# Kernel optimization log

Measured on AMD Instinct MI355X. Metric: run time of the kernel, lower is better.

The kernel has to match this reference:

```python
import jax, jax.numpy as jnp
import numpy as np

D_MODEL = 1024
N_HEADS = 16
D_HEAD = 64
D_MLP = 4096
EPS = 1e-5
IGNORE = -1e5
ATTN_SCALE = float(np.sqrt(D_HEAD))


def setup_inputs() -> dict:
    key = jax.random.key(0)
    ks = jax.random.split(key, 10)
    s = 0.02
    return {
        "x": jax.random.normal(ks[0], (2, 2048, D_MODEL), jnp.float32),
        "ln1_w": jnp.ones((D_MODEL,), jnp.float32),
        "ln1_b": jnp.zeros((D_MODEL,), jnp.float32),
        "W_Q": jax.random.normal(ks[1], (N_HEADS, D_MODEL, D_HEAD), jnp.float32) * s,
        "W_K": jax.random.normal(ks[2], (N_HEADS, D_MODEL, D_HEAD), jnp.float32) * s,
        "W_V": jax.random.normal(ks[3], (N_HEADS, D_MODEL, D_HEAD), jnp.float32) * s,
        "W_O": jax.random.normal(ks[4], (N_HEADS, D_HEAD, D_MODEL), jnp.float32) * s,
        "b_Q": jnp.zeros((N_HEADS, D_HEAD), jnp.float32),
        "b_K": jnp.zeros((N_HEADS, D_HEAD), jnp.float32),
        "b_V": jnp.zeros((N_HEADS, D_HEAD), jnp.float32),
        "b_O": jnp.zeros((D_MODEL,), jnp.float32),
        "ln2_w": jnp.ones((D_MODEL,), jnp.float32),
        "ln2_b": jnp.zeros((D_MODEL,), jnp.float32),
        "W_in": jax.random.normal(ks[5], (D_MODEL, D_MLP), jnp.float32) * s,
        "b_in": jnp.zeros((D_MLP,), jnp.float32),
        "W_out": jax.random.normal(ks[6], (D_MLP, D_MODEL), jnp.float32) * s,
        "b_out": jnp.zeros((D_MODEL,), jnp.float32),
    }


def layer_norm(x, w, b):
    x = x - x.mean(axis=-1, keepdims=True)
    scale = jnp.sqrt((x * x).mean(axis=-1, keepdims=True) + EPS)
    return (x / scale) * w + b


def attention(x, W_Q, W_K, W_V, W_O, b_Q, b_K, b_V, b_O):
    # x: [b, s, d_model]; W_{Q,K,V}: [h, d_model, d_head]
    q = jnp.einsum('bsm,hmd->bshd', x, W_Q) + b_Q
    k = jnp.einsum('bsm,hmd->bshd', x, W_K) + b_K
    v = jnp.einsum('bsm,hmd->bshd', x, W_V) + b_V
    scores = jnp.einsum('bqhd,bkhd->bhqk', q, k) / ATTN_SCALE
    s = x.shape[1]
    mask = jnp.tril(jnp.ones((s, s), bool))  # causal
    scores = jnp.where(mask, scores, IGNORE)
    attn = jax.nn.softmax(scores, axis=-1)
    z = jnp.einsum('bkhd,bhqk->bqhd', v, attn)
    return jnp.einsum('bqhd,hdm->bqm', z, W_O) + b_O


def mlp(x, W_in, b_in, W_out, b_out):
    pre = jnp.einsum('bsm,mf->bsf', x, W_in) + b_in
    post = jax.nn.gelu(pre, approximate=False)
    return jnp.einsum('bsf,fm->bsm', post, W_out) + b_out


def reference(x, ln1_w, ln1_b, W_Q, W_K, W_V, W_O, b_Q, b_K, b_V, b_O,
              ln2_w, ln2_b, W_in, b_in, W_out, b_out):
    resid = x + attention(layer_norm(x, ln1_w, ln1_b), W_Q, W_K, W_V, W_O,
                          b_Q, b_K, b_V, b_O)
    out = resid + mlp(layer_norm(resid, ln2_w, ln2_b), W_in, b_in, W_out, b_out)
    return out
```

## Files before the change

### kernel.cpp

```cpp
#include <hip/hip_runtime.h>

typedef __attribute__((ext_vector_type(4))) float f32x4;
typedef __attribute__((ext_vector_type(8))) __bf16 bf16x8;
typedef __attribute__((ext_vector_type(8))) unsigned short ushort8;
typedef __attribute__((ext_vector_type(4))) unsigned short ushort4v;

union UBF8 { ushort8 u; bf16x8 b; };
static __device__ __forceinline__ bf16x8 as_bf(ushort8 v) { UBF8 x; x.u = v; return x.b; }

static __device__ __forceinline__ unsigned short f2bf(float f) {
  union { __bf16 h; unsigned short u; } v; v.h = (__bf16)f; return v.u;
}

static __device__ __forceinline__ unsigned short f2bf_rn(float f) {
  union { float f; unsigned u; } v; v.f = f;
  unsigned r = v.u + 0x7fffu + ((v.u >> 16) & 1u);
  return (unsigned short)(r >> 16);
}

static __device__ __forceinline__ bf16x8 scale8(ushort8 u, float c) {
  ushort8 r;
#pragma unroll
  for (int j = 0; j < 8; j++) {
    union { unsigned u; float f; } t; t.u = ((unsigned)u[j]) << 16;
    r[j] = f2bf_rn(t.f * c);
  }
  return as_bf(r);
}

static __device__ __forceinline__ float gelu_f(float x) {
  return 0.5f * x * (1.0f + erff(x * 0.70710678118654752f));
}

typedef const __attribute__((address_space(1))) void* gas_p;
typedef __attribute__((address_space(3))) void* las_p;
static __device__ __forceinline__ void gload16(const void* g, void* l) {
  __builtin_amdgcn_global_load_lds((gas_p)g, (las_p)l, 16, 0, 0);
}

__global__ __launch_bounds__(256) void ln_kernel(
    const float* __restrict__ in, const float* __restrict__ w,
    const float* __restrict__ b, unsigned short* __restrict__ out)
{
  const int row = blockIdx.x, t = threadIdx.x;
  const float4 v = *reinterpret_cast<const float4*>(in + (size_t)row * 1024 + t * 4);
  float s = v.x + v.y + v.z + v.w;
#pragma unroll
  for (int o = 32; o >= 1; o >>= 1) s += __shfl_xor(s, o);
  __shared__ float ps[4], qs[4];
  if ((t & 63) == 0) ps[t >> 6] = s;
  __syncthreads();
  const float mean = (ps[0] + ps[1] + ps[2] + ps[3]) * (1.0f / 1024.0f);
  const float cx = v.x - mean, cy = v.y - mean, cz = v.z - mean, cw = v.w - mean;
  float q = cx * cx + cy * cy + cz * cz + cw * cw;
#pragma unroll
  for (int o = 32; o >= 1; o >>= 1) q += __shfl_xor(q, o);
  if ((t & 63) == 0) qs[t >> 6] = q;
  __syncthreads();
  const float rstd = rsqrtf((qs[0] + qs[1] + qs[2] + qs[3]) * (1.0f / 1024.0f) + 1e-5f);
  const float4 wv = *reinterpret_cast<const float4*>(w + t * 4);
  const float4 bv = *reinterpret_cast<const float4*>(b + t * 4);
  ushort4v o4;
  o4.x = f2bf(cx * rstd * wv.x + bv.x);
  o4.y = f2bf(cy * rstd * wv.y + bv.y);
  o4.z = f2bf(cz * rstd * wv.z + bv.z);
  o4.w = f2bf(cw * rstd * wv.w + bv.w);
  *reinterpret_cast<ushort4v*>(out + (size_t)row * 1024 + t * 4) = o4;
}

__global__ __launch_bounds__(256) void conv_qkv_kernel(
    const float* __restrict__ WQ, const float* __restrict__ WK,
    const float* __restrict__ WV, unsigned short* __restrict__ out)
{
  __shared__ float t[32][33];
  const int mat_h = blockIdx.z;
  const int mat = mat_h >> 4, h = mat_h & 15;
  const float* W = (mat == 0 ? WQ : (mat == 1 ? WK : WV)) + (size_t)h * (1024 * 64);
  const int m0 = blockIdx.x * 32;
  const int d0 = blockIdx.y * 32;
  const int tx = threadIdx.x & 31, ty = threadIdx.x >> 5;
#pragma unroll
  for (int j = 0; j < 4; j++)
    t[ty + j * 8][tx] = W[(size_t)(m0 + ty + j * 8) * 64 + d0 + tx];
  __syncthreads();
  const size_t obase = (size_t)(mat * 1024 + h * 64 + d0);
#pragma unroll
  for (int j = 0; j < 4; j++)
    out[(obase + ty + j * 8) * 1024 + m0 + tx] = f2bf(t[tx][ty + j * 8]);
}

__global__ __launch_bounds__(256) void pack_bias_kernel(
    const float* __restrict__ bQ, const float* __restrict__ bK,
    const float* __restrict__ bV, float* __restrict__ out)
{
  const int i = blockIdx.x * 256 + threadIdx.x;
  if (i < 1024) out[i] = bQ[i];
  else if (i < 2048) out[i] = bK[i - 1024];
  else if (i < 3072) out[i] = bV[i - 2048];
}

__global__ __launch_bounds__(256) void transpose_cast_kernel(
    const float* __restrict__ in, unsigned short* __restrict__ out, int R, int C)
{
  __shared__ float t[32][33];
  const int c0 = blockIdx.x * 32, r0 = blockIdx.y * 32;
  const int tx = threadIdx.x & 31, ty = threadIdx.x >> 5;
#pragma unroll
  for (int j = 0; j < 4; j++)
    t[ty + j * 8][tx] = in[(size_t)(r0 + ty + j * 8) * C + c0 + tx];
  __syncthreads();
#pragma unroll
  for (int j = 0; j < 4; j++)
    out[(size_t)(c0 + ty + j * 8) * R + r0 + tx] = f2bf(t[tx][ty + j * 8]);
}

template <int BN, int EPI, int WAVES>
__global__ __launch_bounds__(WAVES * 64) void gemm_kernel(
    const unsigned short* __restrict__ A, const unsigned short* __restrict__ Bt,
    void* Cout, const float* __restrict__ bias, const float* resid,
    int N, int K, int gx)
{
  constexpr int BM = 128, BK = 64;
  constexpr int NF = (BN * 2) / (WAVES * 16);
  constexpr int CA = (BM / 8) / WAVES;
  constexpr int CB = (BN / 8) / WAVES;
  __shared__ __align__(16) unsigned short As[2][BM * BK];
  __shared__ __align__(16) unsigned short Bs[2][BN * BK];
  const int tid = threadIdx.x, lane = tid & 63, w = tid >> 6;
  const int nwg = gridDim.x;
  int id = blockIdx.x;
  id = (id & 7) * (nwg >> 3) + (id >> 3);
  const int bm = (id % gx) * BM, bn = (id / gx) * BN;

  const int l15 = lane & 15, hi = lane >> 4;
  const int arow = (w >> 2) * 64;
  const int brow = (w & 3) * (BN / 4);
  f32x4 acc[4][NF] = {};

  const int srow = lane >> 3;
  const int scol = ((lane & 7) ^ srow) * 8;
  const unsigned short* Ag[CA];
  const unsigned short* Bg[CB];
#pragma unroll
  for (int it = 0; it < CA; it++)
    Ag[it] = A + (size_t)(bm + 8 * (it * WAVES + w) + srow) * K + scol;
#pragma unroll
  for (int it = 0; it < CB; it++)
    Bg[it] = Bt + (size_t)(bn + 8 * (it * WAVES + w) + srow) * K + scol;

  const int rsw = (l15 & 7) << 4;
  const int NT = K / BK;

  auto stage = [&](int k0, int buf) {
#pragma unroll
    for (int it = 0; it < CA; it++)
      gload16(Ag[it] + k0, &As[buf][(it * WAVES + w) * 512]);
#pragma unroll
    for (int it = 0; it < CB; it++)
      gload16(Bg[it] + k0, &Bs[buf][(it * WAVES + w) * 512]);
  };

  stage(0, 0);
  __syncthreads();
  int cur = 0;

  for (int t = 0; t < NT; ++t) {
    if (t + 1 < NT) stage((t + 1) * BK, cur ^ 1);

    const char* Asb = (const char*)As[cur];
    const char* Bsb = (const char*)Bs[cur];
    bf16x8 af[2][4], bfr[2][NF];
#pragma unroll
    for (int kk = 0; kk < 2; kk++) {
      const int cb = kk * 64 + hi * 16;
#pragma unroll
      for (int mf = 0; mf < 4; mf++) {
        const int R = arow + mf * 16 + l15;
        af[kk][mf] = as_bf(*reinterpret_cast<const ushort8*>(Asb + R * (BK * 2) + (cb ^ rsw)));
      }
#pragma unroll
      for (int nf = 0; nf < NF; nf++) {
        const int R = brow + nf * 16 + l15;
        bfr[kk][nf] = as_bf(*reinterpret_cast<const ushort8*>(Bsb + R * (BK * 2) + (cb ^ rsw)));
      }
    }
#pragma unroll
    for (int kk = 0; kk < 2; kk++)
#pragma unroll
      for (int mf = 0; mf < 4; mf++)
#pragma unroll
        for (int nf = 0; nf < NF; nf++)
          acc[mf][nf] = __builtin_amdgcn_mfma_f32_16x16x32_bf16(af[kk][mf], bfr[kk][nf], acc[mf][nf], 0, 0, 0);

    __syncthreads();
    cur ^= 1;
  }

  const int row0 = bm + arow + 4 * hi;
  const int col0 = bn + brow + l15;
#pragma unroll
  for (int mf = 0; mf < 4; mf++) {
#pragma unroll
    for (int nf = 0; nf < NF; nf++) {
#pragma unroll
      for (int i = 0; i < 4; i++) {
        const int row = row0 + mf * 16 + i;
        const int col = col0 + nf * 16;
        float v = acc[mf][nf][i] + bias[col];
        if (EPI == 1) v += resid[(size_t)row * N + col];
        if (EPI == 2) v = gelu_f(v);
        if (EPI == 1) ((float*)Cout)[(size_t)row * N + col] = v;
        else          ((unsigned short*)Cout)[(size_t)row * N + col] = f2bf(v);
      }
    }
  }
}

__global__ __launch_bounds__(256) void attn_kernel(
    const unsigned short* __restrict__ qkv, unsigned short* __restrict__ zout)
{
  __shared__ __align__(16) unsigned short Ks[64 * 72];
  __shared__ __align__(16) unsigned short Vt[64 * 72];
  __shared__ __align__(16) unsigned short Ps[4 * 16 * 72];
  const int tid = threadIdx.x, lane = tid & 63, w = tid >> 6;
  const int l15 = lane & 15, hi = lane >> 4, ko = hi * 8;
  const int j = blockIdx.x, bh = blockIdx.y;
  const int cA = j, cB = 31 - j;
  const size_t tok0 = (size_t)(bh >> 4) * 2048;
  const int h = bh & 15;
  const int qoff = h * 64, koff = 1024 + h * 64, voff = 2048 + h * 64;
  const int rowA = cA * 64 + w * 16;
  const int rowB = cB * 64 + w * 16;
  const float qscale = 0.125f * 1.44269504f;

  bf16x8 qfA[2], qfB[2];
#pragma unroll
  for (int kf = 0; kf < 2; kf++) {
    qfA[kf] = scale8(*reinterpret_cast<const ushort8*>(qkv + (tok0 + rowA + l15) * 3072 + qoff + kf * 32 + ko), qscale);
    qfB[kf] = scale8(*reinterpret_cast<const ushort8*>(qkv + (tok0 + rowB + l15) * 3072 + qoff + kf * 32 + ko), qscale);
  }

  float mA[4], lA[4], mB[4], lB[4];
  f32x4 zA[4], zB[4];
#pragma unroll
  for (int i = 0; i < 4; i++) {
    mA[i] = -1e30f; lA[i] = 0.0f; mB[i] = -1e30f; lB[i] = 0.0f;
#pragma unroll
    for (int nf = 0; nf < 4; nf++) { zA[nf][i] = 0.0f; zB[nf][i] = 0.0f; }
  }

  unsigned short* Pw = Ps + w * (16 * 72);
  const int sr = tid >> 3, scol = (tid & 7) * 8;

  for (int kt = 0; kt <= cB; kt++) {
    __syncthreads();
#pragma unroll
    for (int it = 0; it < 2; it++) {
      const int rr = sr + it * 32;
      const size_t gb = (tok0 + kt * 64 + rr) * 3072;
      *reinterpret_cast<ushort8*>(&Ks[rr * 72 + scol]) =
          *reinterpret_cast<const ushort8*>(qkv + gb + koff + scol);
      ushort8 vv = *reinterpret_cast<const ushort8*>(qkv + gb + voff + scol);
#pragma unroll
      for (int jj = 0; jj < 8; jj++) {
        const int d = scol + jj;
        Vt[d * 72 + (rr ^ (((d >> 3) & 7) << 3))] = vv[jj];
      }
    }
    __syncthreads();

    bf16x8 kb[4][2], vb[4][2];
#pragma unroll
    for (int nf = 0; nf < 4; nf++)
#pragma unroll
      for (int kf = 0; kf < 2; kf++) {
        kb[nf][kf] = as_bf(*reinterpret_cast<const ushort8*>(&Ks[(nf * 16 + l15) * 72 + kf * 32 + ko]));
        const int d = nf * 16 + l15;
        vb[nf][kf] = as_bf(*reinterpret_cast<const ushort8*>(
            &Vt[d * 72 + ((kf * 32 + ko) ^ (((d >> 3) & 7) << 3))]));
      }

    const bool actA = (kt <= cA);

    f32x4 sA[4] = {}, sB[4] = {};
    __builtin_amdgcn_s_setprio(1);
#pragma unroll
    for (int nf = 0; nf < 4; nf++)
#pragma unroll
      for (int kf = 0; kf < 2; kf++) {
        if (actA) sA[nf] = __builtin_amdgcn_mfma_f32_16x16x32_bf16(qfA[kf], kb[nf][kf], sA[nf], 0, 0, 0);
        sB[nf] = __builtin_amdgcn_mfma_f32_16x16x32_bf16(qfB[kf], kb[nf][kf], sB[nf], 0, 0, 0);
      }
    __builtin_amdgcn_s_setprio(0);

    auto process = [&](f32x4* s, float* mrow, float* lrow, f32x4* accz, int rowbase, bool dm) {
#pragma unroll
      for (int i = 0; i < 4; i++) {
        const int rg = rowbase + 4 * hi + i;
        float mx = -1e30f;
#pragma unroll
        for (int nf = 0; nf < 4; nf++) {
          float v = s[nf][i];
          if (dm && (kt * 64 + nf * 16 + l15 > rg)) v = -1e30f;
          s[nf][i] = v;
          mx = fmaxf(mx, v);
        }
#pragma unroll
        for (int o = 1; o <= 8; o <<= 1) mx = fmaxf(mx, __shfl_xor(mx, o));
        const float mnew = fmaxf(mrow[i], mx);
        const float fct = exp2f(mrow[i] - mnew);
        mrow[i] = mnew;
        float rs = 0.0f;
#pragma unroll
        for (int nf = 0; nf < 4; nf++) {
          const float pv = exp2f(s[nf][i] - mnew);
          s[nf][i] = pv;
          rs += pv;
        }
#pragma unroll
        for (int o = 1; o <= 8; o <<= 1) rs += __shfl_xor(rs, o);
        lrow[i] = lrow[i] * fct + rs;
#pragma unroll
        for (int nf = 0; nf < 4; nf++) accz[nf][i] *= fct;
      }
#pragma unroll
      for (int i = 0; i < 4; i++)
#pragma unroll
        for (int nf = 0; nf < 4; nf++)
          Pw[(4 * hi + i) * 72 + ((nf * 16 + l15) ^ (hi << 3))] = f2bf_rn(s[nf][i]);
#pragma unroll
      for (int kf = 0; kf < 2; kf++) {
        const bf16x8 pa = as_bf(*reinterpret_cast<const ushort8*>(
            &Pw[l15 * 72 + ((kf * 32 + ko) ^ (((l15 >> 2) & 3) << 3))]));
        __builtin_amdgcn_s_setprio(1);
#pragma unroll
        for (int nf = 0; nf < 4; nf++)
          accz[nf] = __builtin_amdgcn_mfma_f32_16x16x32_bf16(pa, vb[nf][kf], accz[nf], 0, 0, 0);
        __builtin_amdgcn_s_setprio(0);
      }
    };

    if (actA) process(sA, mA, lA, zA, rowA, kt >= cA);
    process(sB, mB, lB, zB, rowB, kt >= cB);
  }

  auto wb = [&](float* lrow, f32x4* accz, int rowbase) {
#pragma unroll
    for (int i = 0; i < 4; i++) {
      const float inv = 1.0f / lrow[i];
      const int srow = rowbase + 4 * hi + i;
#pragma unroll
      for (int nf = 0; nf < 4; nf++)
        zout[(tok0 + srow) * 1024 + h * 64 + nf * 16 + l15] = f2bf_rn(accz[nf][i] * inv);
    }
  };
  wb(lA, zA, rowA);
  wb(lB, zB, rowB);
}

extern "C" void kernel_launch(void* const* d_in, const int* in_sizes, int n_in,
                              void* d_out, int out_size, void* d_ws, size_t ws_size,
                              hipStream_t stream)
{
  const float* x    = (const float*)d_in[0];
  const float* ln1w = (const float*)d_in[1];
  const float* ln1b = (const float*)d_in[2];
  const float* WQ   = (const float*)d_in[3];
  const float* WK   = (const float*)d_in[4];
  const float* WV   = (const float*)d_in[5];
  const float* WO   = (const float*)d_in[6];
  const float* bQ   = (const float*)d_in[7];
  const float* bK   = (const float*)d_in[8];
  const float* bV   = (const float*)d_in[9];
  const float* bO   = (const float*)d_in[10];
  const float* ln2w = (const float*)d_in[11];
  const float* ln2b = (const float*)d_in[12];
  const float* Win  = (const float*)d_in[13];
  const float* bin  = (const float*)d_in[14];
  const float* Wout = (const float*)d_in[15];
  const float* bout = (const float*)d_in[16];
  float* out = (float*)d_out;

  char* ws = (char*)d_ws;
  unsigned short* bufA   = (unsigned short*)ws;
  unsigned short* bufB   = (unsigned short*)(ws + (size_t)(32 << 20));
  unsigned short* bufC   = (unsigned short*)(ws + (size_t)(40 << 20));
  float*          biasQKV = (float*)(ws + (size_t)(48 << 20));

  ln_kernel<<<4096, 256, 0, stream>>>(x, ln1w, ln1b, bufB);
  conv_qkv_kernel<<<dim3(32, 2, 48), 256, 0, stream>>>(WQ, WK, WV, bufC);
  pack_bias_kernel<<<12, 256, 0, stream>>>(bQ, bK, bV, biasQKV);
  gemm_kernel<128, 0, 8><<<768, 512, 0, stream>>>(bufB, bufC, bufA, biasQKV, nullptr, 3072, 1024, 32);
  attn_kernel<<<dim3(16, 32), 256, 0, stream>>>(bufA, bufB);
  transpose_cast_kernel<<<dim3(32, 32), 256, 0, stream>>>(WO, bufC, 1024, 1024);
  gemm_kernel<64, 1, 8><<<512, 512, 0, stream>>>(bufB, bufC, out, bO, x, 1024, 1024, 32);
  ln_kernel<<<4096, 256, 0, stream>>>(out, ln2w, ln2b, bufB);
  transpose_cast_kernel<<<dim3(128, 32), 256, 0, stream>>>(Win, bufC, 1024, 4096);
  gemm_kernel<128, 2, 8><<<1024, 512, 0, stream>>>(bufB, bufC, bufA, bin, nullptr, 4096, 1024, 32);
  transpose_cast_kernel<<<dim3(32, 128), 256, 0, stream>>>(Wout, bufC, 4096, 1024);
  gemm_kernel<64, 1, 8><<<512, 512, 0, stream>>>(bufA, bufC, out, bout, out, 1024, 4096, 32);
}
```

Before: 292.5 us.

## Split attention KV loop across two blocks and merge partials in combine kernel

Each attention block now handles only even or odd key tiles, which doubles the grid from 512 to 1024 blocks and raises occupancy and latency hiding. Each half writes unnormalized bf16 partial outputs plus per-row max and sum, using the output buffer and a small workspace region as scratch. A new combine kernel rescales and merges the two partials in log-sum-exp fashion before the output projection. The cost is an extra launch, roughly 24MB of additional memory traffic, and one more bf16 rounding of the unnormalized partials.

```diff
diff --git a/kernel.cpp b/kernel.cpp
--- a/kernel.cpp
+++ b/kernel.cpp
@@ -18,13 +18,14 @@
   return (unsigned short)(r >> 16);
 }
 
+static __device__ __forceinline__ float bf2f(unsigned short u) {
+  union { unsigned u; float f; } t; t.u = ((unsigned)u) << 16; return t.f;
+}
+
 static __device__ __forceinline__ bf16x8 scale8(ushort8 u, float c) {
   ushort8 r;
 #pragma unroll
-  for (int j = 0; j < 8; j++) {
-    union { unsigned u; float f; } t; t.u = ((unsigned)u[j]) << 16;
-    r[j] = f2bf_rn(t.f * c);
-  }
+  for (int j = 0; j < 8; j++) r[j] = f2bf_rn(bf2f(u[j]) * c);
   return as_bf(r);
 }
 
@@ -217,14 +218,16 @@
 }
 
 __global__ __launch_bounds__(256) void attn_kernel(
-    const unsigned short* __restrict__ qkv, unsigned short* __restrict__ zout)
+    const unsigned short* __restrict__ qkv, unsigned short* __restrict__ pp,
+    float* __restrict__ ml)
 {
   __shared__ __align__(16) unsigned short Ks[64 * 72];
   __shared__ __align__(16) unsigned short Vt[64 * 72];
   __shared__ __align__(16) unsigned short Ps[4 * 16 * 72];
   const int tid = threadIdx.x, lane = tid & 63, w = tid >> 6;
   const int l15 = lane & 15, hi = lane >> 4, ko = hi * 8;
-  const int j = blockIdx.x, bh = blockIdx.y;
+  const int j = blockIdx.x >> 1, par = blockIdx.x & 1;
+  const int bh = blockIdx.y;
   const int cA = j, cB = 31 - j;
   const size_t tok0 = (size_t)(bh >> 4) * 2048;
   const int h = bh & 15;
@@ -252,7 +255,7 @@
   unsigned short* Pw = Ps + w * (16 * 72);
   const int sr = tid >> 3, scol = (tid & 7) * 8;
 
-  for (int kt = 0; kt <= cB; kt++) {
+  for (int kt = par; kt <= cB; kt += 2) {
     __syncthreads();
 #pragma unroll
     for (int it = 0; it < 2; it++) {
@@ -344,18 +347,47 @@
     process(sB, mB, lB, zB, rowB, kt >= cB);
   }
 
-  auto wb = [&](float* lrow, f32x4* accz, int rowbase) {
+  unsigned short* ppb = pp + (size_t)par * 4194304;
+  float* Mp = ml + par * 131072;
+  float* Lp = Mp + 65536;
+  auto wb = [&](float* mrow, float* lrow, f32x4* accz, int rowbase) {
 #pragma unroll
     for (int i = 0; i < 4; i++) {
-      const float inv = 1.0f / lrow[i];
       const int srow = rowbase + 4 * hi + i;
+      const size_t gtok = tok0 + srow;
 #pragma unroll
       for (int nf = 0; nf < 4; nf++)
-        zout[(tok0 + srow) * 1024 + h * 64 + nf * 16 + l15] = f2bf_rn(accz[nf][i] * inv);
+        ppb[gtok * 1024 + h * 64 + nf * 16 + l15] = f2bf_rn(accz[nf][i]);
+      if (l15 == 0) {
+        const int idx = (int)gtok * 16 + h;
+        Mp[idx] = mrow[i];
+        Lp[idx] = lrow[i];
+      }
     }
   };
-  wb(lA, zA, rowA);
-  wb(lB, zB, rowB);
+  wb(mA, lA, zA, rowA);
+  wb(mB, lB, zB, rowB);
+}
+
+__global__ __launch_bounds__(256) void attn_combine(
+    const unsigned short* __restrict__ pp, const float* __restrict__ ml,
+    unsigned short* __restrict__ zout)
+{
+  const int tok = blockIdx.x, t = threadIdx.x;
+#pragma unroll
+  for (int k = 0; k < 4; k++) {
+    const int col = k * 256 + t;
+    const int h = col >> 6;
+    const int idx = tok * 16 + h;
+    const float m0 = ml[idx],           l0 = ml[65536 + idx];
+    const float m1 = ml[131072 + idx],  l1 = ml[131072 + 65536 + idx];
+    const float mx = fmaxf(m0, m1);
+    const float s0 = exp2f(m0 - mx), s1 = exp2f(m1 - mx);
+    const float p0 = bf2f(pp[(size_t)tok * 1024 + col]);
+    const float p1 = bf2f(pp[4194304 + (size_t)tok * 1024 + col]);
+    const float z = (p0 * s0 + p1 * s1) / (l0 * s0 + l1 * s1);
+    zout[(size_t)tok * 1024 + col] = f2bf_rn(z);
+  }
 }
 
 extern "C" void kernel_launch(void* const* d_in, const int* in_sizes, int n_in,
@@ -383,6 +415,7 @@
 
   char* ws = (char*)d_ws;
   unsigned short* bufA   = (unsigned short*)ws;
+  float*          mlbuf  = (float*)(ws + (size_t)(26 << 20));
   unsigned short* bufB   = (unsigned short*)(ws + (size_t)(32 << 20));
   unsigned short* bufC   = (unsigned short*)(ws + (size_t)(40 << 20));
   float*          biasQKV = (float*)(ws + (size_t)(48 << 20));
@@ -391,7 +424,8 @@
   conv_qkv_kernel<<<dim3(32, 2, 48), 256, 0, stream>>>(WQ, WK, WV, bufC);
   pack_bias_kernel<<<12, 256, 0, stream>>>(bQ, bK, bV, biasQKV);
   gemm_kernel<128, 0, 8><<<768, 512, 0, stream>>>(bufB, bufC, bufA, biasQKV, nullptr, 3072, 1024, 32);
-  attn_kernel<<<dim3(16, 32), 256, 0, stream>>>(bufA, bufB);
+  attn_kernel<<<dim3(32, 32), 256, 0, stream>>>(bufA, (unsigned short*)d_out, mlbuf);
+  attn_combine<<<4096, 256, 0, stream>>>((const unsigned short*)d_out, mlbuf, bufB);
   transpose_cast_kernel<<<dim3(32, 32), 256, 0, stream>>>(WO, bufC, 1024, 1024);
   gemm_kernel<64, 1, 8><<<512, 512, 0, stream>>>(bufB, bufC, out, bO, x, 1024, 1024, 32);
   ln_kernel<<<4096, 256, 0, stream>>>(out, ln2w, ln2b, bufB);
```

New measurement: 305.4 us. 1.04x slower.
